# Kernel optimization log

Hardware: AMD Instinct MI355X
Metric: run time of the kernel (lower is better)

The kernel has to match this reference:

```python
import jax, jax.numpy as jnp
import numpy as np
import math

B, T, C = 2, 2048, 2048
NH, HS = 16, 128
NLQ, NLKV, DHR = 512, 512, 64

def _rope(x, cos, sin):
    # x: [B,T,H,D]; pairs rotated two-at-a-time as in apply_rotary_emb
    b, t, h, d = x.shape
    xr = x.reshape(b, t, h, d // 2, 2)
    re, im = xr[..., 0], xr[..., 1]
    c = cos[None, :, None, :]
    s = sin[None, :, None, :]
    out = jnp.stack([re * c - im * s, re * s + im * c], axis=-1)
    return out.reshape(b, t, h, d)

def setup_inputs() -> dict:
    key = jax.random.key(0)
    ks = jax.random.split(key, 12)
    pos = jnp.arange(T, dtype=jnp.float32)[:, None]
    inv = 1.0 / (10000.0 ** (jnp.arange(0, DHR, 2, dtype=jnp.float32) / DHR))
    ang = pos * inv[None, :]  # [T, DHR//2]
    sc = 0.02
    return {
        "x": jax.random.normal(ks[0], (B, T, C), jnp.float32),
        "cos": jnp.cos(ang),
        "sin": jnp.sin(ang),
        "W_dq": jax.random.normal(ks[1], (NLQ, C), jnp.float32) * sc,
        "W_uq": jax.random.normal(ks[2], (C, NLQ), jnp.float32) * sc,
        "W_dkv": jax.random.normal(ks[3], (NLKV, C), jnp.float32) * sc,
        "W_uk": jax.random.normal(ks[4], (C, NLKV), jnp.float32) * sc,
        "W_uv": jax.random.normal(ks[5], (C, NLKV), jnp.float32) * sc,
        "W_qr": jax.random.normal(ks[6], (NH * DHR, NLQ), jnp.float32) * sc,
        "W_kr": jax.random.normal(ks[7], (DHR, C), jnp.float32) * sc,
        "W_o": jax.random.normal(ks[8], (C, C), jnp.float32) * sc,
    }

def reference(x, cos, sin, W_dq, W_uq, W_dkv, W_uk, W_uv, W_qr, W_kr, W_o):
    b, t, c = x.shape
    # query latent
    c_q = x @ W_dq.T  # [B,T,NLQ]
    # absorbed matrices (training path of FullMHLA)
    k_eff = jnp.einsum('hqs,hsk->hqk',
                       W_uq.reshape(NLQ, NH, HS).transpose(1, 0, 2),
                       W_uk.reshape(NH, HS, NLKV))  # [NH,NLQ,NLKV]
    v_eff = (W_uv.T @ W_o.T).reshape(NLKV, NH, HS).transpose(1, 0, 2)  # [NH,NLKV,HS]
    # kv latent
    c_kv = x @ W_dkv.T  # [B,T,NLKV]
    # content scores: c_q @ k_eff @ c_kv^T
    q_lat = jnp.einsum('btq,hqk->bhtk', c_q, k_eff)          # [B,NH,T,NLKV]
    attn_c = jnp.einsum('bhtk,bsk->bhts', q_lat, c_kv)       # [B,NH,T,T]
    # decoupled RoPE scores
    k_r = _rope((x @ W_kr.T)[:, :, None, :], cos, sin)[:, :, 0, :]  # [B,T,DHR]
    q_r = _rope((c_q @ W_qr.T).reshape(b, t, NH, DHR), cos, sin)    # [B,T,NH,DHR]
    attn_r = jnp.einsum('bthd,bsd->bhts', q_r, k_r)
    attn = (attn_c + attn_r) / math.sqrt(HS + DHR)
    causal = jnp.tril(jnp.ones((t, t), dtype=bool))
    attn = jnp.where(causal[None, None], attn, -jnp.inf)
    attn = jax.nn.softmax(attn, axis=-1)
    # output: attn @ c_kv @ v_eff  (W_o absorbed into v_eff)
    ctx = jnp.einsum('bhts,bsk->bhtk', attn, c_kv)
    y = jnp.einsum('bhtk,hkd->bthd', ctx, v_eff).reshape(b, t, c)
    return y
```

## Files before the change

kernel.cpp:

```cpp
#include <hip/hip_runtime.h>


typedef __bf16 bf16;
typedef __bf16 bf16x8 __attribute__((ext_vector_type(8)));
typedef __bf16 bf16x4 __attribute__((ext_vector_type(4)));
typedef float f32x4 __attribute__((ext_vector_type(4)));
typedef unsigned short u16x4v __attribute__((ext_vector_type(4)));
typedef unsigned short u16x8v __attribute__((ext_vector_type(8)));

#define MFMA16(a, b, c) __builtin_amdgcn_mfma_f32_16x16x32_bf16((a), (b), (c), 0, 0, 0)

__device__ __forceinline__ void stage16(const bf16* g, bf16* lds)
{
    __builtin_amdgcn_global_load_lds(
        (const __attribute__((address_space(1))) unsigned int*)g,
        (__attribute__((address_space(3))) unsigned int*)lds,
        16, 0, 0);
}

__device__ __forceinline__ void tr_pair(unsigned addr, u16x4v& lo, u16x4v& hi)
{
    asm volatile("ds_read_b64_tr_b16 %0, %2\n\t"
                 "ds_read_b64_tr_b16 %1, %2 offset:128"
                 : "=&v"(lo), "=&v"(hi)
                 : "v"(addr)
                 : "memory");
}

__device__ __forceinline__ bf16x8 bv8(u16x4v lo, u16x4v hi)
{
    u16x8v u = __builtin_shufflevector(lo, hi, 0, 1, 2, 3, 4, 5, 6, 7);
    return __builtin_bit_cast(bf16x8, u);
}

struct CvtDesc { const float* src; bf16* dst; long long n4; };
struct CvtArgs { CvtDesc d[9]; };

__global__ void convert_many(CvtArgs a)
{
    CvtDesc d = a.d[blockIdx.y];
    long long i = (long long)blockIdx.x * blockDim.x + threadIdx.x;
    long long stride = (long long)gridDim.x * blockDim.x;
    for (; i < d.n4; i += stride) {
        f32x4 v = ((const f32x4*)d.src)[i];
        bf16x4 o;
        o[0] = (bf16)v[0]; o[1] = (bf16)v[1]; o[2] = (bf16)v[2]; o[3] = (bf16)v[3];
        ((bf16x4*)d.dst)[i] = o;
    }
}

template <typename OutT>
__global__ __launch_bounds__(256, 4)
void gemm_nt(const bf16* __restrict__ A, const bf16* __restrict__ B,
             OutT* __restrict__ C, int K, int lda, int ldb, int ldc,
             long long sAb, long long sAh, long long sBb, long long sBh,
             long long sCb, long long sCh, int ZH)
{
    __shared__ __attribute__((aligned(16))) bf16 As[64 * 32];
    __shared__ __attribute__((aligned(16))) bf16 Bs[64 * 32];

    int z = blockIdx.z;
    int bb = z / ZH, hh = z % ZH;
    A += bb * sAb + hh * sAh;
    B += bb * sBb + hh * sBh;
    C += bb * sCb + hh * sCh;

    int tid = threadIdx.x;
    int w = tid >> 6, lane = tid & 63, l16 = lane & 15, quad = lane >> 4;
    int m0 = blockIdx.x * 64;
    int n0 = blockIdx.y * 64;

    int srow = w * 16 + (lane >> 2);
    int scol = (lane & 3) * 8;
    const bf16* gA = A + (long long)(m0 + srow) * lda + scol;
    const bf16* gB = B + (long long)(n0 + srow) * ldb + scol;
    bf16* lA = As + w * 512;
    bf16* lB = Bs + w * 512;

    const bf16* fA = As + (w * 16 + l16) * 32 + quad * 8;
    f32x4 acc[4] = {};

    for (int k = 0; k < K; k += 32) {
        __syncthreads();
        stage16(gA + k, lA);
        stage16(gB + k, lB);
        __syncthreads();

        bf16x8 a = *(const bf16x8*)fA;
#pragma unroll
        for (int nt = 0; nt < 4; ++nt) {
            bf16x8 b = *(const bf16x8*)(Bs + (nt * 16 + l16) * 32 + quad * 8);
            acc[nt] = MFMA16(a, b, acc[nt]);
        }
    }
#pragma unroll
    for (int nt = 0; nt < 4; ++nt)
#pragma unroll
        for (int r = 0; r < 4; ++r) {
            int row = m0 + w * 16 + quad * 4 + r;
            int col = n0 + nt * 16 + l16;
            C[(long long)row * ldc + col] = (OutT)acc[nt][r];
        }
}

template <typename OutT>
__global__ __launch_bounds__(256, 2)
void gemm_nt128(const bf16* __restrict__ A, const bf16* __restrict__ B,
                OutT* __restrict__ C, int K, int lda, int ldb, int ldc,
                long long sAb, long long sAh, long long sBb, long long sBh,
                long long sCb, long long sCh, int ZH)
{
    __shared__ __attribute__((aligned(16))) bf16 As[128 * 32];
    __shared__ __attribute__((aligned(16))) bf16 Bs[128 * 32];

    int z = blockIdx.z;
    int bb = z / ZH, hh = z % ZH;
    A += bb * sAb + hh * sAh;
    B += bb * sBb + hh * sBh;
    C += bb * sCb + hh * sCh;

    int tid = threadIdx.x;
    int w = tid >> 6, lane = tid & 63, l16 = lane & 15, quad = lane >> 4;
    int wr = w >> 1, wc = w & 1;
    int m0 = blockIdx.x * 128;
    int n0 = blockIdx.y * 128;

    int srow = lane >> 2;
    int scol = (lane & 3) * 8;
    const bf16* gA = A + (long long)(m0 + srow) * lda + scol;
    const bf16* gB = B + (long long)(n0 + srow) * ldb + scol;

    f32x4 acc[4][4] = {};

    for (int k = 0; k < K; k += 32) {
        __syncthreads();
#pragma unroll
        for (int j = 0; j < 2; ++j) {
            int c = j * 4 + w;
            stage16(gA + (long long)(c * 16) * lda + k, As + c * 512);
            stage16(gB + (long long)(c * 16) * ldb + k, Bs + c * 512);
        }
        __syncthreads();

        bf16x8 a[4], b[4];
#pragma unroll
        for (int t = 0; t < 4; ++t) {
            a[t] = *(const bf16x8*)(As + (wr * 64 + t * 16 + l16) * 32 + quad * 8);
            b[t] = *(const bf16x8*)(Bs + (wc * 64 + t * 16 + l16) * 32 + quad * 8);
        }
#pragma unroll
        for (int mt = 0; mt < 4; ++mt)
#pragma unroll
            for (int nt = 0; nt < 4; ++nt)
                acc[mt][nt] = MFMA16(a[mt], b[nt], acc[mt][nt]);
    }
#pragma unroll
    for (int mt = 0; mt < 4; ++mt)
#pragma unroll
        for (int nt = 0; nt < 4; ++nt)
#pragma unroll
            for (int r = 0; r < 4; ++r) {
                int row = m0 + wr * 64 + mt * 16 + quad * 4 + r;
                int col = n0 + wc * 64 + nt * 16 + l16;
                C[(long long)row * ldc + col] = (OutT)acc[mt][nt][r];
            }
}

__global__ __launch_bounds__(256, 4)
void gemm_nn(const bf16* __restrict__ A, const bf16* __restrict__ B,
             bf16* __restrict__ C, int K, int lda, int ldb, int ldc,
             long long sAb, long long sAh, long long sBb, long long sBh,
             long long sCb, long long sCh, int ZH)
{
    __shared__ __attribute__((aligned(16))) bf16 BTs[2048];

    int z = blockIdx.z;
    int bb = z / ZH, hh = z % ZH;
    A += bb * sAb + hh * sAh;
    B += bb * sBb + hh * sBh;
    C += bb * sCb + hh * sCh;

    int tid = threadIdx.x;
    int w = tid >> 6, lane = tid & 63, l16 = lane & 15, quad = lane >> 4;
    int m0 = blockIdx.x * 64;
    int n0 = blockIdx.y * 64;

    int srow = (lane >> 3) * 4 + ((lane >> 1) & 3);
    int scol = (lane & 1) * 8;
    const bf16* gB = B + (long long)srow * ldb + n0 + w * 16 + scol;
    bf16* lB = BTs + w * 512;

    const bf16* Arow = A + (long long)(m0 + w * 16 + l16) * lda;
    unsigned trb = (unsigned)(unsigned long long)(const void*)BTs
                 + (unsigned)(quad * 256 + l16 * 8);

    f32x4 acc[4] = {};

    for (int k = 0; k < K; k += 32) {
        __syncthreads();
        stage16(gB + (long long)k * ldb, lB);
        __syncthreads();

        bf16x8 a = *(const bf16x8*)(Arow + k + quad * 8);
        u16x4v L0, H0, L1, H1, L2, H2, L3, H3;
        tr_pair(trb,        L0, H0);
        tr_pair(trb + 1024, L1, H1);
        tr_pair(trb + 2048, L2, H2);
        tr_pair(trb + 3072, L3, H3);
        asm volatile("s_waitcnt lgkmcnt(0)" ::: "memory");
        __builtin_amdgcn_sched_barrier(0);
        acc[0] = MFMA16(a, bv8(L0, H0), acc[0]);
        acc[1] = MFMA16(a, bv8(L1, H1), acc[1]);
        acc[2] = MFMA16(a, bv8(L2, H2), acc[2]);
        acc[3] = MFMA16(a, bv8(L3, H3), acc[3]);
    }
#pragma unroll
    for (int nt = 0; nt < 4; ++nt)
#pragma unroll
        for (int r = 0; r < 4; ++r) {
            int row = m0 + w * 16 + quad * 4 + r;
            int col = n0 + nt * 16 + l16;
            C[(long long)row * ldc + col] = (bf16)acc[nt][r];
        }
}

__global__ __launch_bounds__(256, 2)
void gemm_nn128(const bf16* __restrict__ A, const bf16* __restrict__ B,
                bf16* __restrict__ C, int K, int lda, int ldb, int ldc,
                long long sAb, long long sAh, long long sBb, long long sBh,
                long long sCb, long long sCh, int ZH)
{
    __shared__ __attribute__((aligned(16))) bf16 As[128 * 32];
    __shared__ __attribute__((aligned(16))) bf16 BTs[4096];

    int z = blockIdx.z;
    int bb = z / ZH, hh = z % ZH;
    A += bb * sAb + hh * sAh;
    B += bb * sBb + hh * sBh;
    C += bb * sCb + hh * sCh;

    int tid = threadIdx.x;
    int w = tid >> 6, lane = tid & 63, l16 = lane & 15, quad = lane >> 4;
    int wr = w >> 1, wc = w & 1;
    int m0 = blockIdx.x * 128;
    int n0 = blockIdx.y * 128;

    int sArow = lane >> 2;
    int sAcol = (lane & 3) * 8;
    const bf16* gA = A + (long long)(m0 + sArow) * lda + sAcol;

    int sBrow = (lane >> 3) * 4 + ((lane >> 1) & 3);
    int sBcol = (lane & 1) * 8;
    const bf16* gB = B + (long long)sBrow * ldb + n0 + sBcol;

    unsigned trb = (unsigned)(unsigned long long)(const void*)BTs
                 + (unsigned)(quad * 256 + l16 * 8);

    f32x4 acc[4][4] = {};

    for (int k = 0; k < K; k += 32) {
        __syncthreads();
#pragma unroll
        for (int j = 0; j < 2; ++j) {
            int c = j * 4 + w;
            stage16(gA + (long long)(c * 16) * lda + k, As + c * 512);
            stage16(gB + (long long)k * ldb + c * 16, BTs + c * 512);
        }
        __syncthreads();

        bf16x8 a[4];
#pragma unroll
        for (int mt = 0; mt < 4; ++mt)
            a[mt] = *(const bf16x8*)(As + (wr * 64 + mt * 16 + l16) * 32 + quad * 8);

        u16x4v L0, H0, L1, H1, L2, H2, L3, H3;
        unsigned tb = trb + (unsigned)(wc * 4096);
        tr_pair(tb,        L0, H0);
        tr_pair(tb + 1024, L1, H1);
        tr_pair(tb + 2048, L2, H2);
        tr_pair(tb + 3072, L3, H3);
        asm volatile("s_waitcnt lgkmcnt(0)" ::: "memory");
        __builtin_amdgcn_sched_barrier(0);
        bf16x8 b[4] = { bv8(L0, H0), bv8(L1, H1), bv8(L2, H2), bv8(L3, H3) };
#pragma unroll
        for (int mt = 0; mt < 4; ++mt)
#pragma unroll
            for (int nt = 0; nt < 4; ++nt)
                acc[mt][nt] = MFMA16(a[mt], b[nt], acc[mt][nt]);
    }
#pragma unroll
    for (int mt = 0; mt < 4; ++mt)
#pragma unroll
        for (int nt = 0; nt < 4; ++nt)
#pragma unroll
            for (int r = 0; r < 4; ++r) {
                int row = m0 + wr * 64 + mt * 16 + quad * 4 + r;
                int col = n0 + wc * 64 + nt * 16 + l16;
                C[(long long)row * ldc + col] = (bf16)acc[mt][nt][r];
            }
}

__global__ void rope_k_kernel(const bf16* __restrict__ krr, const float* __restrict__ cosb,
                              const float* __restrict__ sinb, bf16* __restrict__ Kcat)
{
    int i = blockIdx.x * 256 + threadIdx.x;
    int pr = i & 31;
    int row = i >> 5;
    int t = row & 2047;
    float re = (float)krr[row * 64 + 2 * pr];
    float im = (float)krr[row * 64 + 2 * pr + 1];
    float c = cosb[t * 32 + pr];
    float s = sinb[t * 32 + pr];
    long long base = (long long)row * 576 + 512 + 2 * pr;
    Kcat[base]     = (bf16)(re * c - im * s);
    Kcat[base + 1] = (bf16)(re * s + im * c);
}

__global__ void rope_q_kernel(const bf16* __restrict__ qrr, const float* __restrict__ cosb,
                              const float* __restrict__ sinb, bf16* __restrict__ Qcat)
{
    int i = blockIdx.x * 256 + threadIdx.x;
    int pr = i & 31;
    int h = (i >> 5) & 15;
    int t = (i >> 9) & 2047;
    int b = i >> 20;
    long long src = ((long long)(b * 2048 + t)) * 1024 + h * 64 + 2 * pr;
    float re = (float)qrr[src];
    float im = (float)qrr[src + 1];
    float c = cosb[t * 32 + pr];
    float s = sinb[t * 32 + pr];
    long long dst = ((long long)((b * 16 + h) * 2048 + t)) * 576 + 512 + 2 * pr;
    Qcat[dst]     = (bf16)(re * c - im * s);
    Qcat[dst + 1] = (bf16)(re * s + im * c);
}

#define ATTN_SCALE 0.07216878364870322f

__global__ __launch_bounds__(256, 2)
void flash_mla(const bf16* __restrict__ Qcat, const bf16* __restrict__ Kcat,
               bf16* __restrict__ ctx)
{
    __shared__ __attribute__((aligned(16))) bf16 KT[288 * 64];
    __shared__ __attribute__((aligned(16))) bf16 P[4][16 * 40];

    const int T = 2048;
    int z = blockIdx.y;
    int b = z >> 4;
    int bx = blockIdx.x;
    int tid = threadIdx.x;
    int w = tid >> 6, lane = tid & 63, l16 = lane & 15, quad = lane >> 4;

    const bf16* Qb = Qcat + (long long)z * T * 576;
    const bf16* Kb = Kcat + (long long)b * T * 576;
    bf16* Ob = ctx + (long long)z * T * 512;

    int srow = (lane >> 3) * 4 + ((lane >> 1) & 3);
    int scol = (lane & 1) * 8;

    const bf16* kq0 = KT + ((quad >> 1) * 8 + (l16 >> 2)) * 64
                         + (l16 & 3) * 16 + (quad & 1) * 8;

    unsigned trbase = (unsigned)(unsigned long long)(const void*)KT
                    + (unsigned)(quad * 256 + l16 * 8);

    for (int strip = 0; strip < 2; ++strip) {
        int qt = strip == 0 ? bx : 31 - bx;
        int qbase = qt * 64;
        const bf16* Qrow = Qb + (long long)(qbase + w * 16 + l16) * 576;

        f32x4 o[32] = {};
        float mrow[4], lrow[4];
#pragma unroll
        for (int r = 0; r < 4; ++r) { mrow[r] = -1e30f; lrow[r] = 0.f; }

        int ntiles = (qbase + 64) >> 5;
        for (int st = 0; st < ntiles; ++st) {
            int s0 = st << 5;

            __syncthreads();
            {
                const bf16* gs = Kb + (long long)(s0 + srow) * 576 + scol;
#pragma unroll
                for (int it = 0; it < 9; ++it) {
                    int ci = it * 4 + w;
                    stage16(gs + ci * 16, KT + ci * 512);
                }
            }
            __syncthreads();

            f32x4 sa = {0.f, 0.f, 0.f, 0.f}, sb = {0.f, 0.f, 0.f, 0.f};
            __builtin_amdgcn_s_setprio(1);
#pragma unroll
            for (int kk = 0; kk < 18; ++kk) {
                bf16x8 a  = *(const bf16x8*)(Qrow + kk * 32 + quad * 8);
                bf16x8 b0 = *(const bf16x8*)(kq0 + kk * 1024);
                bf16x8 b1 = *(const bf16x8*)(kq0 + kk * 1024 + 256);
                sa = MFMA16(a, b0, sa);
                sb = MFMA16(a, b1, sb);
            }
            __builtin_amdgcn_s_setprio(0);

            float alpha[4];
#pragma unroll
            for (int r = 0; r < 4; ++r) {
                int trow = qbase + w * 16 + quad * 4 + r;
                float v0 = sa[r] * ATTN_SCALE;
                float v1 = sb[r] * ATTN_SCALE;
                if (s0 + l16 > trow)      v0 = -1e30f;
                if (s0 + 16 + l16 > trow) v1 = -1e30f;
                float rm = fmaxf(v0, v1);
#pragma unroll
                for (int off = 1; off < 16; off <<= 1)
                    rm = fmaxf(rm, __shfl_xor(rm, off, 64));
                float mnew = fmaxf(mrow[r], rm);
                alpha[r] = __expf(mrow[r] - mnew);
                mrow[r] = mnew;
                float p0 = __expf(v0 - mnew);
                float p1 = __expf(v1 - mnew);
                float rs = p0 + p1;
#pragma unroll
                for (int off = 1; off < 16; off <<= 1)
                    rs += __shfl_xor(rs, off, 64);
                lrow[r] = lrow[r] * alpha[r] + rs;
                P[w][(quad * 4 + r) * 40 + l16]      = (bf16)p0;
                P[w][(quad * 4 + r) * 40 + 16 + l16] = (bf16)p1;
            }

            bf16x8 pa = *(const bf16x8*)(&P[w][l16 * 40 + quad * 8]);
            asm volatile("s_waitcnt lgkmcnt(0)" ::: "memory");
            __builtin_amdgcn_sched_barrier(0);

            u16x4v L[2], H[2];
            tr_pair(trbase, L[0], H[0]);
            __builtin_amdgcn_s_setprio(1);
#pragma unroll
            for (int nt = 0; nt < 32; ++nt) {
                if (nt < 31) {
                    tr_pair(trbase + (unsigned)((nt + 1) * 1024), L[(nt + 1) & 1], H[(nt + 1) & 1]);
                    asm volatile("s_waitcnt lgkmcnt(2)" ::: "memory");
                } else {
                    asm volatile("s_waitcnt lgkmcnt(0)" ::: "memory");
                }
                __builtin_amdgcn_sched_barrier(0);
#pragma unroll
                for (int r = 0; r < 4; ++r) o[nt][r] *= alpha[r];
                o[nt] = MFMA16(pa, bv8(L[nt & 1], H[nt & 1]), o[nt]);
            }
            __builtin_amdgcn_s_setprio(0);
        }

#pragma unroll
        for (int nt = 0; nt < 32; ++nt)
#pragma unroll
            for (int r = 0; r < 4; ++r) {
                int trow = qbase + w * 16 + quad * 4 + r;
                Ob[(long long)trow * 512 + nt * 16 + l16] = (bf16)(o[nt][r] / lrow[r]);
            }
    }
}

extern "C" void kernel_launch(void* const* d_in, const int* in_sizes, int n_in,
                              void* d_out, int out_size, void* d_ws, size_t ws_size,
                              hipStream_t stream)
{
    const float* xf    = (const float*)d_in[0];
    const float* cosb  = (const float*)d_in[1];
    const float* sinb  = (const float*)d_in[2];
    const float* Wdqf  = (const float*)d_in[3];
    const float* Wuqf  = (const float*)d_in[4];
    const float* Wdkvf = (const float*)d_in[5];
    const float* Wukf  = (const float*)d_in[6];
    const float* Wuvf  = (const float*)d_in[7];
    const float* Wqrf  = (const float*)d_in[8];
    const float* Wkrf  = (const float*)d_in[9];
    const float* Wof   = (const float*)d_in[10];
    float* y = (float*)d_out;

    char* ws = (char*)d_ws;
    bf16* c_q  = (bf16*)ws; ws += (size_t)4096 * 512 * 2;
    bf16* Kcat = (bf16*)ws; ws += (size_t)4096 * 576 * 2;
    bf16* krr  = (bf16*)ws; ws += (size_t)4096 * 64 * 2;
    bf16* qrr  = (bf16*)ws; ws += (size_t)4096 * 1024 * 2;
    bf16* vC2  = (bf16*)ws; ws += (size_t)2048 * 512 * 2;
    bf16* keff = (bf16*)ws; ws += (size_t)16 * 512 * 512 * 2;
    bf16* Qcat = (bf16*)ws; ws += (size_t)32 * 2048 * 576 * 2;
    bf16* ctx  = (bf16*)ws; ws += (size_t)32 * 2048 * 512 * 2;
    bf16* x    = (bf16*)ws; ws += (size_t)4096 * 2048 * 2;
    bf16* Wdq  = (bf16*)ws; ws += (size_t)512 * 2048 * 2;
    bf16* Wuq  = (bf16*)ws; ws += (size_t)2048 * 512 * 2;
    bf16* Wdkv = (bf16*)ws; ws += (size_t)512 * 2048 * 2;
    bf16* Wuk  = (bf16*)ws; ws += (size_t)2048 * 512 * 2;
    bf16* Wuv  = (bf16*)ws; ws += (size_t)2048 * 512 * 2;
    bf16* Wqr  = (bf16*)ws; ws += (size_t)1024 * 512 * 2;
    bf16* Wkr  = (bf16*)ws; ws += (size_t)64 * 2048 * 2;
    bf16* Wo   = (bf16*)ws; ws += (size_t)2048 * 2048 * 2;

    dim3 blk(256);

    CvtArgs ca;
    ca.d[0] = {xf,    x,    (long long)4096 * 2048 / 4};
    ca.d[1] = {Wdqf,  Wdq,  (long long)512 * 2048 / 4};
    ca.d[2] = {Wuqf,  Wuq,  (long long)2048 * 512 / 4};
    ca.d[3] = {Wdkvf, Wdkv, (long long)512 * 2048 / 4};
    ca.d[4] = {Wukf,  Wuk,  (long long)2048 * 512 / 4};
    ca.d[5] = {Wuvf,  Wuv,  (long long)2048 * 512 / 4};
    ca.d[6] = {Wqrf,  Wqr,  (long long)1024 * 512 / 4};
    ca.d[7] = {Wkrf,  Wkr,  (long long)64 * 2048 / 4};
    ca.d[8] = {Wof,   Wo,   (long long)2048 * 2048 / 4};
    convert_many<<<dim3(512, 9), blk, 0, stream>>>(ca);

    gemm_nt<bf16><<<dim3(64, 8, 1), blk, 0, stream>>>(x, Wdq, c_q, 2048, 2048, 2048, 512,
                                                      0, 0, 0, 0, 0, 0, 1);
    gemm_nt<bf16><<<dim3(64, 8, 1), blk, 0, stream>>>(x, Wdkv, Kcat, 2048, 2048, 2048, 576,
                                                      0, 0, 0, 0, 0, 0, 1);
    gemm_nt<bf16><<<dim3(64, 1, 1), blk, 0, stream>>>(x, Wkr, krr, 2048, 2048, 2048, 64,
                                                      0, 0, 0, 0, 0, 0, 1);
    gemm_nt<bf16><<<dim3(64, 16, 1), blk, 0, stream>>>(c_q, Wqr, qrr, 512, 512, 512, 1024,
                                                       0, 0, 0, 0, 0, 0, 1);
    gemm_nn<<<dim3(32, 8, 1), blk, 0, stream>>>(Wo, Wuv, vC2, 2048, 2048, 512, 512,
                                                0, 0, 0, 0, 0, 0, 1);
    gemm_nn<<<dim3(8, 8, 16), blk, 0, stream>>>(Wuq, Wuk, keff, 128, 2048, 512, 512,
                                                0, 128, 0, 65536, 0, 262144, 16);
    gemm_nn128<<<dim3(16, 4, 32), blk, 0, stream>>>(c_q, keff, Qcat, 512, 512, 512, 576,
                                                    (long long)2048 * 512, 0,
                                                    0, 262144,
                                                    (long long)16 * 2048 * 576,
                                                    (long long)2048 * 576, 16);
    rope_k_kernel<<<dim3(512), blk, 0, stream>>>(krr, cosb, sinb, Kcat);
    rope_q_kernel<<<dim3(16384), blk, 0, stream>>>(qrr, cosb, sinb, Qcat);
    flash_mla<<<dim3(16, 32), blk, 0, stream>>>(Qcat, Kcat, ctx);
    gemm_nt128<float><<<dim3(16, 1, 32), blk, 0, stream>>>(ctx, vC2, y, 512, 512, 512, 2048,
                                                           (long long)16 * 2048 * 512,
                                                           (long long)2048 * 512,
                                                           0, 65536,
                                                           (long long)2048 * 2048, 128, 16);
}
```

Measured before the change: 644.9 us.

## Widen flash-MLA key tile to 64 and add lazy softmax rescaling

The key/value tile in the flash attention loop grows from 32 to 64 rows, which doubles the LDS staging buffer and the P buffer and issues two PV MFMAs per output column tile. This halves the number of barrier-synchronised staging iterations per strip and amortises the softmax and shuffle work over more keys. It also adds a deferred-rescale path: when no row's max grows by more than 8, the running max is kept and the alpha rescale of the 32 accumulators is skipped. The cost is larger LDS use (about 74KB plus P), which may limit the two-blocks-per-CU occupancy, and more register pressure.

```diff
diff --git a/kernel.cpp b/kernel.cpp
--- a/kernel.cpp
+++ b/kernel.cpp
@@ -340,8 +340,8 @@
 void flash_mla(const bf16* __restrict__ Qcat, const bf16* __restrict__ Kcat,
                bf16* __restrict__ ctx)
 {
-    __shared__ __attribute__((aligned(16))) bf16 KT[288 * 64];
-    __shared__ __attribute__((aligned(16))) bf16 P[4][16 * 40];
+    __shared__ __attribute__((aligned(16))) bf16 KT[576 * 64];
+    __shared__ __attribute__((aligned(16))) bf16 P[4][16 * 64];
 
     const int T = 2048;
     int z = blockIdx.y;
@@ -357,7 +357,7 @@
     int srow = (lane >> 3) * 4 + ((lane >> 1) & 3);
     int scol = (lane & 1) * 8;
 
-    const bf16* kq0 = KT + ((quad >> 1) * 8 + (l16 >> 2)) * 64
+    const bf16* kq0 = KT + ((quad >> 1) * 16 + (l16 >> 2)) * 64
                          + (l16 & 3) * 16 + (quad & 1) * 8;
 
     unsigned trbase = (unsigned)(unsigned long long)(const void*)KT
@@ -373,78 +373,109 @@
 #pragma unroll
         for (int r = 0; r < 4; ++r) { mrow[r] = -1e30f; lrow[r] = 0.f; }
 
-        int ntiles = (qbase + 64) >> 5;
+        int ntiles = qt + 1;
         for (int st = 0; st < ntiles; ++st) {
-            int s0 = st << 5;
+            int s0 = st << 6;
 
             __syncthreads();
             {
-                const bf16* gs = Kb + (long long)(s0 + srow) * 576 + scol;
-#pragma unroll
-                for (int it = 0; it < 9; ++it) {
-                    int ci = it * 4 + w;
-                    stage16(gs + ci * 16, KT + ci * 512);
+                const bf16* gs0 = Kb + (long long)(s0 + srow) * 576 + scol;
+                const bf16* gs1 = gs0 + 32 * 576;
+#pragma unroll
+                for (int it = 0; it < 18; ++it) {
+                    int idx = it * 4 + w;
+                    int ci = idx >> 1, h = idx & 1;
+                    stage16((h ? gs1 : gs0) + ci * 16, KT + idx * 512);
                 }
             }
             __syncthreads();
 
-            f32x4 sa = {0.f, 0.f, 0.f, 0.f}, sb = {0.f, 0.f, 0.f, 0.f};
+            f32x4 s4[4] = {};
             __builtin_amdgcn_s_setprio(1);
 #pragma unroll
             for (int kk = 0; kk < 18; ++kk) {
-                bf16x8 a  = *(const bf16x8*)(Qrow + kk * 32 + quad * 8);
-                bf16x8 b0 = *(const bf16x8*)(kq0 + kk * 1024);
-                bf16x8 b1 = *(const bf16x8*)(kq0 + kk * 1024 + 256);
-                sa = MFMA16(a, b0, sa);
-                sb = MFMA16(a, b1, sb);
+                bf16x8 a = *(const bf16x8*)(Qrow + kk * 32 + quad * 8);
+                const bf16* kb = kq0 + kk * 2048;
+#pragma unroll
+                for (int nt2 = 0; nt2 < 4; ++nt2)
+                    s4[nt2] = MFMA16(a, *(const bf16x8*)(kb + nt2 * 256), s4[nt2]);
             }
             __builtin_amdgcn_s_setprio(0);
 
-            float alpha[4];
+            float vv[4][4], rm4[4];
 #pragma unroll
             for (int r = 0; r < 4; ++r) {
                 int trow = qbase + w * 16 + quad * 4 + r;
-                float v0 = sa[r] * ATTN_SCALE;
-                float v1 = sb[r] * ATTN_SCALE;
-                if (s0 + l16 > trow)      v0 = -1e30f;
-                if (s0 + 16 + l16 > trow) v1 = -1e30f;
-                float rm = fmaxf(v0, v1);
+                float rm = -1e30f;
+#pragma unroll
+                for (int nt2 = 0; nt2 < 4; ++nt2) {
+                    float v = s4[nt2][r] * ATTN_SCALE;
+                    if (s0 + nt2 * 16 + l16 > trow) v = -1e30f;
+                    vv[r][nt2] = v;
+                    rm = fmaxf(rm, v);
+                }
 #pragma unroll
                 for (int off = 1; off < 16; off <<= 1)
                     rm = fmaxf(rm, __shfl_xor(rm, off, 64));
-                float mnew = fmaxf(mrow[r], rm);
-                alpha[r] = __expf(mrow[r] - mnew);
-                mrow[r] = mnew;
-                float p0 = __expf(v0 - mnew);
-                float p1 = __expf(v1 - mnew);
-                float rs = p0 + p1;
+                rm4[r] = rm;
+            }
+            bool dfr = true;
+#pragma unroll
+            for (int r = 0; r < 4; ++r) dfr = dfr && (rm4[r] - mrow[r] <= 8.f);
+            bool allDefer = __all(dfr);
+
+            float alpha[4];
+            if (!allDefer) {
+#pragma unroll
+                for (int r = 0; r < 4; ++r) {
+                    float mnew = fmaxf(mrow[r], rm4[r]);
+                    alpha[r] = __expf(mrow[r] - mnew);
+                    mrow[r] = mnew;
+                }
+            }
+#pragma unroll
+            for (int r = 0; r < 4; ++r) {
+                float rs = 0.f;
+#pragma unroll
+                for (int nt2 = 0; nt2 < 4; ++nt2) {
+                    float p = __expf(vv[r][nt2] - mrow[r]);
+                    rs += p;
+                    P[w][(quad * 4 + r) * 64 + nt2 * 16 + l16] = (bf16)p;
+                }
 #pragma unroll
                 for (int off = 1; off < 16; off <<= 1)
                     rs += __shfl_xor(rs, off, 64);
-                lrow[r] = lrow[r] * alpha[r] + rs;
-                P[w][(quad * 4 + r) * 40 + l16]      = (bf16)p0;
-                P[w][(quad * 4 + r) * 40 + 16 + l16] = (bf16)p1;
-            }
-
-            bf16x8 pa = *(const bf16x8*)(&P[w][l16 * 40 + quad * 8]);
+                lrow[r] = (allDefer ? lrow[r] : lrow[r] * alpha[r]) + rs;
+            }
+            if (!allDefer) {
+#pragma unroll
+                for (int nt = 0; nt < 32; ++nt)
+#pragma unroll
+                    for (int r = 0; r < 4; ++r) o[nt][r] *= alpha[r];
+            }
+
+            bf16x8 pa0 = *(const bf16x8*)(&P[w][l16 * 64 + quad * 8]);
+            bf16x8 pa1 = *(const bf16x8*)(&P[w][l16 * 64 + 32 + quad * 8]);
             asm volatile("s_waitcnt lgkmcnt(0)" ::: "memory");
             __builtin_amdgcn_sched_barrier(0);
 
-            u16x4v L[2], H[2];
-            tr_pair(trbase, L[0], H[0]);
+            u16x4v L[2][2], H[2][2];
+            tr_pair(trbase,        L[0][0], H[0][0]);
+            tr_pair(trbase + 1024, L[0][1], H[0][1]);
             __builtin_amdgcn_s_setprio(1);
 #pragma unroll
             for (int nt = 0; nt < 32; ++nt) {
                 if (nt < 31) {
-                    tr_pair(trbase + (unsigned)((nt + 1) * 1024), L[(nt + 1) & 1], H[(nt + 1) & 1]);
-                    asm volatile("s_waitcnt lgkmcnt(2)" ::: "memory");
+                    unsigned tb = trbase + (unsigned)((nt + 1) * 2048);
+                    tr_pair(tb,        L[(nt + 1) & 1][0], H[(nt + 1) & 1][0]);
+                    tr_pair(tb + 1024, L[(nt + 1) & 1][1], H[(nt + 1) & 1][1]);
+                    asm volatile("s_waitcnt lgkmcnt(4)" ::: "memory");
                 } else {
                     asm volatile("s_waitcnt lgkmcnt(0)" ::: "memory");
                 }
                 __builtin_amdgcn_sched_barrier(0);
-#pragma unroll
-                for (int r = 0; r < 4; ++r) o[nt][r] *= alpha[r];
-                o[nt] = MFMA16(pa, bv8(L[nt & 1], H[nt & 1]), o[nt]);
+                o[nt] = MFMA16(pa0, bv8(L[nt & 1][0], H[nt & 1][0]), o[nt]);
+                o[nt] = MFMA16(pa1, bv8(L[nt & 1][1], H[nt & 1][1]), o[nt]);
             }
             __builtin_amdgcn_s_setprio(0);
         }
```

After: 839.9 us. 1.3x slower.
